# Optimization experiments

Measured on AMD Instinct MI355X. Metric: run time of the kernel, lower is better.

Reference implementation:

```python
import jax, jax.numpy as jnp
import numpy as np

BS, C_IN, S1 = 64, 256, 32
D_OUT, J = 32, 10          # out_dim, num_out_caps (as_final_output -> spatial_size_2)
I = S1 * S1                # num_in_caps = 1024
ROUTE_NUM = 3


def setup_inputs() -> dict:
    key = jax.random.key(0)
    k1, k2, k3 = jax.random.split(key, 3)
    x = jax.random.normal(k1, (BS, C_IN, S1, S1), dtype=jnp.float32)
    W = jax.random.normal(k2, (D_OUT * J, C_IN), dtype=jnp.float32) * 0.02  # 1x1 conv weight
    W_b = jax.random.normal(k3, (D_OUT * J,), dtype=jnp.float32) * 0.02     # conv bias
    return {"x": x, "W": W, "W_b": W_b}


def squash(vec):
    # vec: [bs, j, d]; coeff = ||v||^2 / (1+||v||^2) / ||v||
    norm = jnp.linalg.norm(vec, axis=2, keepdims=True)
    norm_sq = norm * norm
    return vec * (norm_sq / (1.0 + norm_sq) / norm)


def reference(x, W, W_b):
    bs = x.shape[0]
    # 1x1 conv == per-pixel matmul: [bs, J*D, h, w]
    pred = jnp.einsum('bchw,oc->bohw', x, W) + W_b[None, :, None, None]
    # torch: resize(bs, J, D, I) on contiguous tensor, then permute(0,3,1,2)
    pred = pred.reshape(bs, J, D_OUT, I).transpose(0, 3, 1, 2)  # [bs, I, J, D]
    b = jnp.zeros((bs, J, I), dtype=x.dtype)  # b_init='zero'
    v = None
    for _ in range(ROUTE_NUM):
        c = jax.nn.softmax(b, axis=1)                    # softmax over output caps j
        s = jnp.einsum('bji,bijd->bjd', c, pred)          # per-capsule weighted sum
        v = squash(s)                                     # [bs, J, D]
        delta_b = jnp.einsum('bjd,bijd->bji', v, pred)    # agreement
        b = b + jax.lax.stop_gradient(delta_b)            # torch .detach()
    return v  # as_final_output=True -> [bs, J, D]
```

## Files before the change

### kernel.cpp

```cpp
#include <hip/hip_runtime.h>
#include <hip/hip_bf16.h>

typedef __attribute__((ext_vector_type(8))) unsigned short u16x8;
typedef __attribute__((ext_vector_type(4))) unsigned short u16x4;
typedef __attribute__((ext_vector_type(8))) short short8;
typedef __attribute__((ext_vector_type(4))) float floatx4;

#define BS 64
#define CIN 256
#define II 1024
#define OO 320
#define JJ 10
#define DD 32

#define DMA16(gsrc, ldst)                                                                 \
    __builtin_amdgcn_global_load_lds((const __attribute__((address_space(1))) void*)(gsrc), \
                                     (__attribute__((address_space(3))) void*)(ldst), 16, 0, 0)

__device__ __forceinline__ float b2f(unsigned short u) {
    union { unsigned int i; float f; } x; x.i = ((unsigned int)u) << 16; return x.f;
}
__device__ __forceinline__ unsigned short f2b(float f) {
    union { float f; unsigned int i; } x; x.f = f;
    unsigned int r = x.i + 0x7fffu + ((x.i >> 16) & 1u);
    return (unsigned short)(r >> 16);
}

__device__ __forceinline__ float butterfly32(const float* p, int l) {
    float q16[16];
#pragma unroll
    for (int d = 0; d < 16; ++d) {
        float keep = (l & 1) ? p[2 * d + 1] : p[2 * d];
        float send = (l & 1) ? p[2 * d] : p[2 * d + 1];
        q16[d] = keep + __shfl_xor(send, 1);
    }
    float q8[8];
#pragma unroll
    for (int d = 0; d < 8; ++d) {
        float keep = (l & 2) ? q16[2 * d + 1] : q16[2 * d];
        float send = (l & 2) ? q16[2 * d] : q16[2 * d + 1];
        q8[d] = keep + __shfl_xor(send, 2);
    }
    float q4[4];
#pragma unroll
    for (int d = 0; d < 4; ++d) {
        float keep = (l & 4) ? q8[2 * d + 1] : q8[2 * d];
        float send = (l & 4) ? q8[2 * d] : q8[2 * d + 1];
        q4[d] = keep + __shfl_xor(send, 4);
    }
    float q2[2];
#pragma unroll
    for (int d = 0; d < 2; ++d) {
        float keep = (l & 8) ? q4[2 * d + 1] : q4[2 * d];
        float send = (l & 8) ? q4[2 * d] : q4[2 * d + 1];
        q2[d] = keep + __shfl_xor(send, 8);
    }
    float keep = (l & 16) ? q2[1] : q2[0];
    float send = (l & 16) ? q2[0] : q2[1];
    float q1 = keep + __shfl_xor(send, 16);
    q1 += __shfl_xor(q1, 32);
    return q1;
}

__global__ __launch_bounds__(256) void k_prepW(const float* __restrict__ W,
                                               unsigned short* __restrict__ Wl) {
    int gid = blockIdx.x * 256 + threadIdx.x;
    int lm = gid & 15;
    int quad = (gid >> 4) & 3;
    int mtl = (gid >> 6) & 3;
    int ks = (gid >> 8) & 7;
    int oc = gid >> 11;
    const float* src = W + (size_t)(oc * 64 + mtl * 16 + lm) * CIN + ks * 32 + quad * 8;
    float4 v0 = *(const float4*)src;
    float4 v1 = *(const float4*)(src + 4);
    u16x8 u;
    u[0] = f2b(v0.x); u[1] = f2b(v0.y); u[2] = f2b(v0.z); u[3] = f2b(v0.w);
    u[4] = f2b(v1.x); u[5] = f2b(v1.y); u[6] = f2b(v1.z); u[7] = f2b(v1.w);
    *(u16x8*)(Wl + (size_t)gid * 8) = u;
}

__global__ __launch_bounds__(512) void k_gemm10(const float* __restrict__ x,
                                                const unsigned short* __restrict__ Wl,
                                                const float* __restrict__ Wb,
                                                unsigned short* __restrict__ pred,
                                                float* __restrict__ psumC) {
    __shared__ unsigned short buf[2][16896];
    __shared__ float Wb_lds[OO];

    const int ic = blockIdx.x, b = blockIdx.y;
    const int t = threadIdx.x, w = t >> 6, l = t & 63;
    const int lm = l & 15, quad = l >> 4;
    const int i0 = ic * 128;

    if (t < OO) Wb_lds[t] = Wb[t];

#pragma unroll
    for (int g = 0; g < 4; ++g)
        DMA16(Wl + (size_t)(t + 512 * g) * 8, &buf[1][(size_t)(t + 512 * g) * 8]);

    short8 bfrag[8];
    float csum[2];
    const int crow = t >> 5, f4 = t & 31;
    const int cs_c = t >> 2, cs_seg = t & 3;
#pragma unroll
    for (int kc = 0; kc < 2; ++kc) {
        float4 fr[8];
#pragma unroll
        for (int p = 0; p < 8; ++p) {
            int c = kc * 128 + p * 16 + crow;
            fr[p] = *(const float4*)(x + ((size_t)b * CIN + c) * II + i0 + 4 * f4);
        }
#pragma unroll
        for (int p = 0; p < 8; ++p) {
            int cl = p * 16 + crow;
            u16x4 u;
            u[0] = f2b(fr[p].x); u[1] = f2b(fr[p].y); u[2] = f2b(fr[p].z); u[3] = f2b(fr[p].w);
            *(u16x4*)&buf[0][cl * 132 + 4 * f4] = u;
        }
        __syncthreads();
#pragma unroll
        for (int k2 = 0; k2 < 4; ++k2) {
            short8 f;
#pragma unroll
            for (int j = 0; j < 8; ++j)
                f[j] = (short)buf[0][(k2 * 32 + quad * 8 + j) * 132 + w * 16 + lm];
            bfrag[kc * 4 + k2] = f;
        }
        {
            float cs = 0.f;
#pragma unroll
            for (int q = 0; q < 8; ++q) {
                u16x4 u = *(const u16x4*)&buf[0][cs_c * 132 + cs_seg * 32 + q * 4];
                cs += b2f(u[0]) + b2f(u[1]) + b2f(u[2]) + b2f(u[3]);
            }
            cs += __shfl_xor(cs, 1);
            cs += __shfl_xor(cs, 2);
            csum[kc] = cs;
        }
        __syncthreads();
    }
    if (cs_seg == 0) {
        size_t cbase = ((size_t)ic * BS + b) * CIN;
        psumC[cbase + cs_c] = csum[0];
        psumC[cbase + 128 + cs_c] = csum[1];
    }

    const size_t predrow = ((size_t)b * II + i0 + w * 16 + lm) * OO;
#pragma unroll 1
    for (int oc = 0; oc < 5; ++oc) {
        if (oc < 4) {
            const unsigned short* src = Wl + (size_t)(oc + 1) * 16384;
#pragma unroll
            for (int g = 0; g < 4; ++g)
                DMA16(src + (size_t)(t + 512 * g) * 8, &buf[oc & 1][(size_t)(t + 512 * g) * 8]);
        }
        const unsigned short* ab = buf[(oc + 1) & 1];
        floatx4 acc[4] = {};
#pragma unroll
        for (int ks = 0; ks < 8; ++ks)
#pragma unroll
            for (int mtl = 0; mtl < 4; ++mtl) {
                short8 af = *(const short8*)(ab + (size_t)(((ks * 4 + mtl) * 4 + quad) * 16 + lm) * 8);
                acc[mtl] = __builtin_amdgcn_mfma_f32_16x16x32_bf16(af, bfrag[ks], acc[mtl], 0, 0, 0);
            }
#pragma unroll
        for (int mtl = 0; mtl < 4; ++mtl) {
            int ob = oc * 64 + mtl * 16 + quad * 4;
            u16x4 sv;
#pragma unroll
            for (int r = 0; r < 4; ++r) sv[r] = f2b(acc[mtl][r] + Wb_lds[ob + r]);
            *(u16x4*)(pred + predrow + ob) = sv;
        }
        __syncthreads();
    }
}

__global__ __launch_bounds__(320) void k_gemv(const float* __restrict__ psumC,
                                              const float* __restrict__ W,
                                              const float* __restrict__ Wb,
                                              float* __restrict__ s1) {
    __shared__ float y_lds[CIN];
    const int b = blockIdx.x, t = threadIdx.x;
    if (t < CIN) {
        float s = 0.f;
#pragma unroll
        for (int sl = 0; sl < 8; ++sl) s += psumC[((size_t)sl * BS + b) * CIN + t];
        y_lds[t] = s;
    }
    __syncthreads();
    const float* wr = W + (size_t)t * CIN;
    float acc = 0.f;
#pragma unroll 4
    for (int c = 0; c < CIN; c += 4) {
        float4 wv = *(const float4*)(wr + c);
        acc += wv.x * y_lds[c] + wv.y * y_lds[c + 1] + wv.z * y_lds[c + 2] + wv.w * y_lds[c + 3];
    }
    s1[(size_t)b * OO + t] = 0.1f * (acc + 1024.0f * Wb[t]);
}

__global__ __launch_bounds__(640) void k_route1(const float* __restrict__ s1,
                                                const unsigned short* __restrict__ pred,
                                                float* __restrict__ blogG,
                                                float* __restrict__ psum1) {
    __shared__ float s_lds[OO];
    __shared__ float v_lds[OO];
    __shared__ float cf[JJ];
    __shared__ float dbuf[JJ][128];

    const int ic = blockIdx.x, b = blockIdx.y;
    const int t = threadIdx.x, w = t >> 6, l = t & 63;

    u16x8 va[4], vb[4];
    {
        const unsigned short* p0 = pred + ((size_t)b * II + ic * 128 + 2 * l) * OO + w * DD;
#pragma unroll
        for (int q = 0; q < 4; ++q) {
            va[q] = *(const u16x8*)(p0 + q * 8);
            vb[q] = *(const u16x8*)(p0 + OO + q * 8);
        }
    }

    if (t < OO) s_lds[t] = s1[(size_t)b * OO + t];
    __syncthreads();
    if (t < JJ) {
        float n2 = 0.f;
#pragma unroll
        for (int d = 0; d < DD; ++d) { float v = s_lds[t * DD + d]; n2 += v * v; }
        cf[t] = sqrtf(n2) / (1.0f + n2);
    }
    __syncthreads();
    if (t < OO) v_lds[t] = s_lds[t] * cf[t >> 5];
    __syncthreads();

    float d0 = 0.f, d1 = 0.f;
#pragma unroll
    for (int q = 0; q < 4; ++q)
#pragma unroll
        for (int e = 0; e < 8; ++e) {
            float vv = v_lds[w * DD + q * 8 + e];
            d0 += vv * b2f(va[q][e]);
            d1 += vv * b2f(vb[q][e]);
        }
    *(float2*)(blogG + ((size_t)b * JJ + w) * II + ic * 128 + 2 * l) = make_float2(d0, d1);
    dbuf[w][2 * l] = d0; dbuf[w][2 * l + 1] = d1;
    __syncthreads();

    if (t < 128) {
        float lg[JJ];
#pragma unroll
        for (int j = 0; j < JJ; ++j) lg[j] = dbuf[j][t];
        float m = lg[0];
#pragma unroll
        for (int j = 1; j < JJ; ++j) m = fmaxf(m, lg[j]);
        float Z = 0.f, c[JJ];
#pragma unroll
        for (int j = 0; j < JJ; ++j) { c[j] = __expf(lg[j] - m); Z += c[j]; }
        float inv = 1.0f / Z;
#pragma unroll
        for (int j = 0; j < JJ; ++j) dbuf[j][t] = c[j] * inv;
    }
    __syncthreads();

    float c0 = dbuf[w][2 * l], c1 = dbuf[w][2 * l + 1];
    float p[DD];
#pragma unroll
    for (int q = 0; q < 4; ++q)
#pragma unroll
        for (int e = 0; e < 8; ++e)
            p[q * 8 + e] = c0 * b2f(va[q][e]) + c1 * b2f(vb[q][e]);
    float s = butterfly32(p, l);
    if (l < 32) psum1[((size_t)ic * BS + b) * OO + w * DD + l] = s;
}

__global__ __launch_bounds__(640) void k_route2(const float* __restrict__ psum1,
                                                const unsigned short* __restrict__ pred,
                                                const float* __restrict__ blogG,
                                                float* __restrict__ psum2) {
    __shared__ float s_lds[OO];
    __shared__ float v_lds[OO];
    __shared__ float cf[JJ];
    __shared__ float dbuf[JJ][128];

    const int ic = blockIdx.x, b = blockIdx.y;
    const int t = threadIdx.x, w = t >> 6, l = t & 63;

    u16x8 va[4], vb[4];
    {
        const unsigned short* p0 = pred + ((size_t)b * II + ic * 128 + 2 * l) * OO + w * DD;
#pragma unroll
        for (int q = 0; q < 4; ++q) {
            va[q] = *(const u16x8*)(p0 + q * 8);
            vb[q] = *(const u16x8*)(p0 + OO + q * 8);
        }
    }

    if (t < OO) {
        float s = 0.f;
#pragma unroll
        for (int sl = 0; sl < 8; ++sl) s += psum1[((size_t)sl * BS + b) * OO + t];
        s_lds[t] = s;
    }
    __syncthreads();
    if (t < JJ) {
        float n2 = 0.f;
#pragma unroll
        for (int d = 0; d < DD; ++d) { float v = s_lds[t * DD + d]; n2 += v * v; }
        cf[t] = sqrtf(n2) / (1.0f + n2);
    }
    __syncthreads();
    if (t < OO) v_lds[t] = s_lds[t] * cf[t >> 5];
    __syncthreads();

    float d0 = 0.f, d1 = 0.f;
#pragma unroll
    for (int q = 0; q < 4; ++q)
#pragma unroll
        for (int e = 0; e < 8; ++e) {
            float vv = v_lds[w * DD + q * 8 + e];
            d0 += vv * b2f(va[q][e]);
            d1 += vv * b2f(vb[q][e]);
        }
    float2 bl = *(const float2*)(blogG + ((size_t)b * JJ + w) * II + ic * 128 + 2 * l);
    dbuf[w][2 * l] = bl.x + d0; dbuf[w][2 * l + 1] = bl.y + d1;
    __syncthreads();

    if (t < 128) {
        float lg[JJ];
#pragma unroll
        for (int j = 0; j < JJ; ++j) lg[j] = dbuf[j][t];
        float m = lg[0];
#pragma unroll
        for (int j = 1; j < JJ; ++j) m = fmaxf(m, lg[j]);
        float Z = 0.f, c[JJ];
#pragma unroll
        for (int j = 0; j < JJ; ++j) { c[j] = __expf(lg[j] - m); Z += c[j]; }
        float inv = 1.0f / Z;
#pragma unroll
        for (int j = 0; j < JJ; ++j) dbuf[j][t] = c[j] * inv;
    }
    __syncthreads();

    float c0 = dbuf[w][2 * l], c1 = dbuf[w][2 * l + 1];
    float p[DD];
#pragma unroll
    for (int q = 0; q < 4; ++q)
#pragma unroll
        for (int e = 0; e < 8; ++e)
            p[q * 8 + e] = c0 * b2f(va[q][e]) + c1 * b2f(vb[q][e]);
    float s = butterfly32(p, l);
    if (l < 32) psum2[((size_t)ic * BS + b) * OO + w * DD + l] = s;
}

__global__ __launch_bounds__(320) void k_final2(const float* __restrict__ psum2,
                                                float* __restrict__ out) {
    __shared__ float s_lds[OO];
    __shared__ float cf[JJ];
    int b = blockIdx.x, t = threadIdx.x;
    float s = 0.f;
#pragma unroll
    for (int sl = 0; sl < 8; ++sl) s += psum2[((size_t)sl * BS + b) * OO + t];
    s_lds[t] = s;
    __syncthreads();
    if (t < JJ) {
        float n2 = 0.f;
#pragma unroll
        for (int d = 0; d < DD; ++d) { float v = s_lds[t * DD + d]; n2 += v * v; }
        cf[t] = sqrtf(n2) / (1.0f + n2);
    }
    __syncthreads();
    out[b * OO + t] = s_lds[t] * cf[t >> 5];
}

extern "C" void kernel_launch(void* const* d_in, const int* in_sizes, int n_in,
                              void* d_out, int out_size, void* d_ws, size_t ws_size,
                              hipStream_t stream) {
    const float* x  = (const float*)d_in[0];
    const float* W  = (const float*)d_in[1];
    const float* Wb = (const float*)d_in[2];

    char* ws = (char*)d_ws;
    unsigned short* pred = (unsigned short*)ws;
    unsigned short* Wl   = (unsigned short*)(ws + 41943040);
    float* psumC = (float*)(ws + 42106880);
    float* s1    = (float*)(ws + 42631168);
    float* psum1 = (float*)(ws + 42713088);
    float* psum2 = (float*)(ws + 43368448);
    float* blogG = (float*)(ws + 44023808);

    k_prepW<<<40, 256, 0, stream>>>(W, Wl);
    k_gemm10<<<dim3(8, BS), 512, 0, stream>>>(x, Wl, Wb, pred, psumC);
    k_gemv<<<BS, 320, 0, stream>>>(psumC, W, Wb, s1);
    k_route1<<<dim3(8, BS), 640, 0, stream>>>(s1, pred, blogG, psum1);
    k_route2<<<dim3(8, BS), 640, 0, stream>>>(psum1, pred, blogG, psum2);
    k_final2<<<BS, 320, 0, stream>>>(psum2, (float*)d_out);
}
```

Before: 154.8 us.

## Fuse weight bf16 conversion into GEMM and GEMV into route1

Drops the separate weight-prep kernel. The GEMM now reads fp32 W directly, converts it to bf16 and writes it to LDS itself, replacing the async global-to-LDS DMA of prepacked weights. The small GEMV kernel is also folded into route1, so each route1 block recomputes s1 for its batch instead of reading it from memory. This removes two kernel launches and some intermediate buffers. In exchange, the weight staging becomes synchronous register-path loads doing twice the bytes, and the GEMV is computed redundantly 8 times per batch.

```diff
diff --git a/kernel.cpp b/kernel.cpp
--- a/kernel.cpp
+++ b/kernel.cpp
@@ -13,10 +13,6 @@
 #define JJ 10
 #define DD 32
 
-#define DMA16(gsrc, ldst)                                                                 \
-    __builtin_amdgcn_global_load_lds((const __attribute__((address_space(1))) void*)(gsrc), \
-                                     (__attribute__((address_space(3))) void*)(ldst), 16, 0, 0)
-
 __device__ __forceinline__ float b2f(unsigned short u) {
     union { unsigned int i; float f; } x; x.i = ((unsigned int)u) << 16; return x.f;
 }
@@ -62,25 +58,24 @@
     return q1;
 }
 
-__global__ __launch_bounds__(256) void k_prepW(const float* __restrict__ W,
-                                               unsigned short* __restrict__ Wl) {
-    int gid = blockIdx.x * 256 + threadIdx.x;
-    int lm = gid & 15;
-    int quad = (gid >> 4) & 3;
-    int mtl = (gid >> 6) & 3;
-    int ks = (gid >> 8) & 7;
-    int oc = gid >> 11;
-    const float* src = W + (size_t)(oc * 64 + mtl * 16 + lm) * CIN + ks * 32 + quad * 8;
-    float4 v0 = *(const float4*)src;
-    float4 v1 = *(const float4*)(src + 4);
-    u16x8 u;
-    u[0] = f2b(v0.x); u[1] = f2b(v0.y); u[2] = f2b(v0.z); u[3] = f2b(v0.w);
-    u[4] = f2b(v1.x); u[5] = f2b(v1.y); u[6] = f2b(v1.z); u[7] = f2b(v1.w);
-    *(u16x8*)(Wl + (size_t)gid * 8) = u;
-}
-
-__global__ __launch_bounds__(512) void k_gemm10(const float* __restrict__ x,
-                                                const unsigned short* __restrict__ Wl,
+__device__ __forceinline__ void stageW(const float* __restrict__ W, unsigned short* dst,
+                                       int oc, int t) {
+#pragma unroll
+    for (int gi = 0; gi < 4; ++gi) {
+        int g = t + 512 * gi;
+        int lm = g & 15, quad = (g >> 4) & 3, mtl = (g >> 6) & 3, ks = g >> 8;
+        const float* src = W + (size_t)(oc * 64 + mtl * 16 + lm) * CIN + ks * 32 + quad * 8;
+        float4 v0 = *(const float4*)src;
+        float4 v1 = *(const float4*)(src + 4);
+        u16x8 u;
+        u[0] = f2b(v0.x); u[1] = f2b(v0.y); u[2] = f2b(v0.z); u[3] = f2b(v0.w);
+        u[4] = f2b(v1.x); u[5] = f2b(v1.y); u[6] = f2b(v1.z); u[7] = f2b(v1.w);
+        *(u16x8*)(dst + (size_t)g * 8) = u;
+    }
+}
+
+__global__ __launch_bounds__(512) void k_gemm11(const float* __restrict__ x,
+                                                const float* __restrict__ W,
                                                 const float* __restrict__ Wb,
                                                 unsigned short* __restrict__ pred,
                                                 float* __restrict__ psumC) {
@@ -94,9 +89,7 @@
 
     if (t < OO) Wb_lds[t] = Wb[t];
 
-#pragma unroll
-    for (int g = 0; g < 4; ++g)
-        DMA16(Wl + (size_t)(t + 512 * g) * 8, &buf[1][(size_t)(t + 512 * g) * 8]);
+    stageW(W, buf[1], 0, t);
 
     short8 bfrag[8];
     float csum[2];
@@ -148,12 +141,7 @@
     const size_t predrow = ((size_t)b * II + i0 + w * 16 + lm) * OO;
 #pragma unroll 1
     for (int oc = 0; oc < 5; ++oc) {
-        if (oc < 4) {
-            const unsigned short* src = Wl + (size_t)(oc + 1) * 16384;
-#pragma unroll
-            for (int g = 0; g < 4; ++g)
-                DMA16(src + (size_t)(t + 512 * g) * 8, &buf[oc & 1][(size_t)(t + 512 * g) * 8]);
-        }
+        if (oc < 4) stageW(W, buf[oc & 1], oc + 1, t);
         const unsigned short* ab = buf[(oc + 1) & 1];
         floatx4 acc[4] = {};
 #pragma unroll
@@ -175,33 +163,13 @@
     }
 }
 
-__global__ __launch_bounds__(320) void k_gemv(const float* __restrict__ psumC,
-                                              const float* __restrict__ W,
-                                              const float* __restrict__ Wb,
-                                              float* __restrict__ s1) {
-    __shared__ float y_lds[CIN];
-    const int b = blockIdx.x, t = threadIdx.x;
-    if (t < CIN) {
-        float s = 0.f;
-#pragma unroll
-        for (int sl = 0; sl < 8; ++sl) s += psumC[((size_t)sl * BS + b) * CIN + t];
-        y_lds[t] = s;
-    }
-    __syncthreads();
-    const float* wr = W + (size_t)t * CIN;
-    float acc = 0.f;
-#pragma unroll 4
-    for (int c = 0; c < CIN; c += 4) {
-        float4 wv = *(const float4*)(wr + c);
-        acc += wv.x * y_lds[c] + wv.y * y_lds[c + 1] + wv.z * y_lds[c + 2] + wv.w * y_lds[c + 3];
-    }
-    s1[(size_t)b * OO + t] = 0.1f * (acc + 1024.0f * Wb[t]);
-}
-
-__global__ __launch_bounds__(640) void k_route1(const float* __restrict__ s1,
+__global__ __launch_bounds__(640) void k_route1(const float* __restrict__ psumC,
+                                                const float* __restrict__ W,
+                                                const float* __restrict__ Wb,
                                                 const unsigned short* __restrict__ pred,
                                                 float* __restrict__ blogG,
                                                 float* __restrict__ psum1) {
+    __shared__ float y_lds[CIN];
     __shared__ float s_lds[OO];
     __shared__ float v_lds[OO];
     __shared__ float cf[JJ];
@@ -220,7 +188,23 @@
         }
     }
 
-    if (t < OO) s_lds[t] = s1[(size_t)b * OO + t];
+    if (t < CIN) {
+        float s = 0.f;
+#pragma unroll
+        for (int sl = 0; sl < 8; ++sl) s += psumC[((size_t)sl * BS + b) * CIN + t];
+        y_lds[t] = s;
+    }
+    __syncthreads();
+    if (t < OO) {
+        const float* wr = W + (size_t)t * CIN;
+        float acc = 0.f;
+#pragma unroll 4
+        for (int c = 0; c < CIN; c += 4) {
+            float4 wv = *(const float4*)(wr + c);
+            acc += wv.x * y_lds[c] + wv.y * y_lds[c + 1] + wv.z * y_lds[c + 2] + wv.w * y_lds[c + 3];
+        }
+        s_lds[t] = 0.1f * (acc + 1024.0f * Wb[t]);
+    }
     __syncthreads();
     if (t < JJ) {
         float n2 = 0.f;
@@ -380,17 +364,13 @@
 
     char* ws = (char*)d_ws;
     unsigned short* pred = (unsigned short*)ws;
-    unsigned short* Wl   = (unsigned short*)(ws + 41943040);
-    float* psumC = (float*)(ws + 42106880);
-    float* s1    = (float*)(ws + 42631168);
-    float* psum1 = (float*)(ws + 42713088);
-    float* psum2 = (float*)(ws + 43368448);
-    float* blogG = (float*)(ws + 44023808);
-
-    k_prepW<<<40, 256, 0, stream>>>(W, Wl);
-    k_gemm10<<<dim3(8, BS), 512, 0, stream>>>(x, Wl, Wb, pred, psumC);
-    k_gemv<<<BS, 320, 0, stream>>>(psumC, W, Wb, s1);
-    k_route1<<<dim3(8, BS), 640, 0, stream>>>(s1, pred, blogG, psum1);
+    float* psumC = (float*)(ws + 41943040);
+    float* psum1 = (float*)(ws + 42467328);
+    float* psum2 = (float*)(ws + 43122688);
+    float* blogG = (float*)(ws + 43778048);
+
+    k_gemm11<<<dim3(8, BS), 512, 0, stream>>>(x, W, Wb, pred, psumC);
+    k_route1<<<dim3(8, BS), 640, 0, stream>>>(psumC, W, Wb, pred, blogG, psum1);
     k_route2<<<dim3(8, BS), 640, 0, stream>>>(psum1, pred, blogG, psum2);
     k_final2<<<BS, 320, 0, stream>>>(psum2, (float*)d_out);
 }
```

New measurement: 172.6 us. 11.5% more time.
